# Kernel optimization log

Measured on AMD Instinct MI355X. Metric: run time of the kernel, lower is better.

Reference implementation:

```python
import jax, jax.numpy as jnp
import numpy as np

B, N, H = 128, 2048, 768
MAX_ANS = 15
NUM_ANS = MAX_ANS + 1  # default ans_to_aid = {str(i): i for i in range(16)}
LN_EPS = 1e-5


def setup_inputs() -> dict:
    key = jax.random.key(0)
    ks = jax.random.split(key, 7)
    s1 = 1.0 / np.sqrt(H)
    s2 = 1.0 / np.sqrt(2 * H)
    return {
        "v_emb": jax.random.normal(ks[0], (B, N, H), dtype=jnp.float32),
        "W1": jax.random.uniform(ks[1], (H, 2 * H), jnp.float32, -s1, s1),
        "b1": jax.random.uniform(ks[2], (2 * H,), jnp.float32, -s1, s1),
        "gamma": jnp.ones((2 * H,), jnp.float32),
        "beta": jnp.zeros((2 * H,), jnp.float32),
        "W2": jax.random.uniform(ks[3], (2 * H, 1), jnp.float32, -s2, s2),
        "b2": jax.random.uniform(ks[4], (1,), jnp.float32, -s2, s2),
    }


def _mlp(v_emb, W1, b1, gamma, beta, W2, b2):
    pooled = jnp.mean(v_emb, axis=1)                      # [B, H]
    h = jnp.dot(pooled, W1) + b1                          # [B, 2H]
    h = jax.nn.gelu(h, approximate=False)                 # torch nn.GELU() exact
    mu = jnp.mean(h, axis=-1, keepdims=True)
    var = jnp.mean((h - mu) ** 2, axis=-1, keepdims=True)
    h = (h - mu) * jax.lax.rsqrt(var + LN_EPS) * gamma + beta
    pred = jnp.dot(h, W2) + b2                            # [B, 1]
    return pred


def _pred_to_logits(pred):
    # vectorized round + clamp + one-hot (replaces per-sample .item() loop)
    aid = jnp.clip(jnp.round(pred[:, 0]), 0, MAX_ANS).astype(jnp.int32)
    return jax.nn.one_hot(aid, NUM_ANS, dtype=jnp.float32)  # [B, NUM_ANS]


def reference(v_emb, W1, b1, gamma, beta, W2, b2):
    pred = _mlp(v_emb, W1, b1, gamma, beta, W2, b2)
    logits = _pred_to_logits(pred)
    return pred, logits
```

## Files before the change

kernel.cpp:

```cpp
#include <hip/hip_runtime.h>
#include <cstdint>
#include <cstddef>

#define BB 128
#define NN 2048
#define HH 768
#define H2 1536
#define SSPLIT 16
#define CHUNK (NN / SSPLIT)
#define RT 16

__global__ __launch_bounds__(192) void pool_kernel(const float* __restrict__ v,
                                                   float* __restrict__ pooled) {
    const int b = blockIdx.x, s = blockIdx.y, t = threadIdx.x;
    const float4* vp =
        reinterpret_cast<const float4*>(v + ((size_t)b * NN + (size_t)s * CHUNK) * HH) + t;
    float4 acc = make_float4(0.f, 0.f, 0.f, 0.f);
#pragma unroll 4
    for (int n = 0; n < CHUNK; ++n) {
        float4 x = vp[(size_t)n * (HH / 4)];
        acc.x += x.x; acc.y += x.y; acc.z += x.z; acc.w += x.w;
    }
    float* p = pooled + (size_t)b * HH + t * 4;
    atomicAdd(p + 0, acc.x);
    atomicAdd(p + 1, acc.y);
    atomicAdd(p + 2, acc.z);
    atomicAdd(p + 3, acc.w);
}

__global__ __launch_bounds__(256) void mlp1_kernel(const float* __restrict__ pooled,
                                                   const float* __restrict__ W1,
                                                   const float* __restrict__ b1,
                                                   float* __restrict__ hbuf) {
    __shared__ float lds[RT * HH];
    const int j0 = blockIdx.x * 256, r0 = blockIdx.y * RT, tid = threadIdx.x;
    const float invN = 1.0f / (float)NN;

    const float4* src = reinterpret_cast<const float4*>(pooled + (size_t)r0 * HH);
    float4* dst = reinterpret_cast<float4*>(lds);
    for (int i = tid; i < RT * HH / 4; i += 256) {
        float4 x = src[i];
        x.x *= invN; x.y *= invN; x.z *= invN; x.w *= invN;
        dst[i] = x;
    }
    __syncthreads();

    const int j = j0 + tid;
    float acc[RT];
#pragma unroll
    for (int r = 0; r < RT; ++r) acc[r] = 0.f;

    const float* w = W1 + j;
    for (int k = 0; k < HH; k += 4) {
        const float w0 = w[(size_t)(k + 0) * H2];
        const float w1 = w[(size_t)(k + 1) * H2];
        const float w2 = w[(size_t)(k + 2) * H2];
        const float w3 = w[(size_t)(k + 3) * H2];
#pragma unroll
        for (int r = 0; r < RT; ++r) {
            float4 p = dst[(r * HH + k) >> 2];
            acc[r] = fmaf(p.x, w0, acc[r]);
            acc[r] = fmaf(p.y, w1, acc[r]);
            acc[r] = fmaf(p.z, w2, acc[r]);
            acc[r] = fmaf(p.w, w3, acc[r]);
        }
    }

    const float bj = b1[j];
#pragma unroll
    for (int r = 0; r < RT; ++r) {
        float hv = acc[r] + bj;
        float g = 0.5f * hv * (1.0f + erff(hv * 0.70710678118654752f));
        hbuf[(size_t)(r0 + r) * H2 + j] = g;
    }
}

__device__ inline float block_sum(float v, float* sbuf, int tid) {
#pragma unroll
    for (int off = 32; off > 0; off >>= 1) v += __shfl_down(v, off, 64);
    if ((tid & 63) == 0) sbuf[tid >> 6] = v;
    __syncthreads();
    if (tid == 0) sbuf[0] = sbuf[0] + sbuf[1] + sbuf[2] + sbuf[3];
    __syncthreads();
    float r = sbuf[0];
    __syncthreads();
    return r;
}

__global__ __launch_bounds__(256) void head_kernel(const float* __restrict__ hbuf,
                                                   const float* __restrict__ gamma,
                                                   const float* __restrict__ beta,
                                                   const float* __restrict__ W2,
                                                   const float* __restrict__ b2,
                                                   float* __restrict__ out) {
    __shared__ float sbuf[4];
    __shared__ int said;
    const int b = blockIdx.x, tid = threadIdx.x;
    const float* row = hbuf + (size_t)b * H2;

    float v[6];
#pragma unroll
    for (int i = 0; i < 6; ++i) v[i] = row[tid + i * 256];

    float s = 0.f;
#pragma unroll
    for (int i = 0; i < 6; ++i) s += v[i];
    const float mu = block_sum(s, sbuf, tid) * (1.0f / (float)H2);

    float sq = 0.f;
#pragma unroll
    for (int i = 0; i < 6; ++i) {
        float d = v[i] - mu;
        sq = fmaf(d, d, sq);
    }
    const float var = block_sum(sq, sbuf, tid) * (1.0f / (float)H2);
    const float rstd = rsqrtf(var + 1e-5f);

    float d = 0.f;
#pragma unroll
    for (int i = 0; i < 6; ++i) {
        int j = tid + i * 256;
        float y = (v[i] - mu) * rstd * gamma[j] + beta[j];
        d = fmaf(y, W2[j], d);
    }
    const float pred = block_sum(d, sbuf, tid) + b2[0];

    if (tid == 0) {
        out[b] = pred;
        float a = rintf(pred);
        a = fminf(fmaxf(a, 0.0f), 15.0f);
        said = (int)a;
    }
    __syncthreads();
    if (tid < 16) out[BB + b * 16 + tid] = (tid == said) ? 1.0f : 0.0f;
}

extern "C" void kernel_launch(void* const* d_in, const int* in_sizes, int n_in,
                              void* d_out, int out_size, void* d_ws, size_t ws_size,
                              hipStream_t stream) {
    const float* v_emb = (const float*)d_in[0];
    const float* W1    = (const float*)d_in[1];
    const float* b1    = (const float*)d_in[2];
    const float* gamma = (const float*)d_in[3];
    const float* beta  = (const float*)d_in[4];
    const float* W2    = (const float*)d_in[5];
    const float* b2    = (const float*)d_in[6];
    float* out = (float*)d_out;

    float* pooled = (float*)d_ws;
    float* hbuf   = pooled + (size_t)BB * HH;

    hipMemsetAsync(d_ws, 0, (size_t)BB * HH * sizeof(float), stream);

    pool_kernel<<<dim3(BB, SSPLIT), 192, 0, stream>>>(v_emb, pooled);
    mlp1_kernel<<<dim3(H2 / 256, BB / RT), 256, 0, stream>>>(pooled, W1, b1, hbuf);
    head_kernel<<<BB, 256, 0, stream>>>(hbuf, gamma, beta, W2, b2, out);
}
```

Measured before the change: 1.120 ms.

## Retile MLP1 to two columns per thread over fewer rows per block

Changes the first dense layer's tiling so each block covers 2 rows and 512 output columns, with each thread computing two columns. The grid grows from 48 blocks to 192 to raise parallelism on the weight-streaming GEMV. The mean scaling moves into the pooling kernel's atomic adds, and the pool loop unroll rises to 8. The trade-off is that W1 is now re-read by many more row blocks, which adds L2 traffic.

```diff
diff --git a/kernel.cpp b/kernel.cpp
--- a/kernel.cpp
+++ b/kernel.cpp
@@ -8,7 +8,8 @@
 #define H2 1536
 #define SSPLIT 16
 #define CHUNK (NN / SSPLIT)
-#define RT 16
+#define RT 2
+#define JT 512
 
 __global__ __launch_bounds__(192) void pool_kernel(const float* __restrict__ v,
                                                    float* __restrict__ pooled) {
@@ -16,62 +17,70 @@
     const float4* vp =
         reinterpret_cast<const float4*>(v + ((size_t)b * NN + (size_t)s * CHUNK) * HH) + t;
     float4 acc = make_float4(0.f, 0.f, 0.f, 0.f);
-#pragma unroll 4
+#pragma unroll 8
     for (int n = 0; n < CHUNK; ++n) {
         float4 x = vp[(size_t)n * (HH / 4)];
         acc.x += x.x; acc.y += x.y; acc.z += x.z; acc.w += x.w;
     }
+    const float invN = 1.0f / (float)NN;
     float* p = pooled + (size_t)b * HH + t * 4;
-    atomicAdd(p + 0, acc.x);
-    atomicAdd(p + 1, acc.y);
-    atomicAdd(p + 2, acc.z);
-    atomicAdd(p + 3, acc.w);
+    atomicAdd(p + 0, acc.x * invN);
+    atomicAdd(p + 1, acc.y * invN);
+    atomicAdd(p + 2, acc.z * invN);
+    atomicAdd(p + 3, acc.w * invN);
 }
 
 __global__ __launch_bounds__(256) void mlp1_kernel(const float* __restrict__ pooled,
                                                    const float* __restrict__ W1,
                                                    const float* __restrict__ b1,
                                                    float* __restrict__ hbuf) {
-    __shared__ float lds[RT * HH];
-    const int j0 = blockIdx.x * 256, r0 = blockIdx.y * RT, tid = threadIdx.x;
-    const float invN = 1.0f / (float)NN;
+    __shared__ float4 lds[RT * HH / 4];
+    const int j0 = blockIdx.x * JT, r0 = blockIdx.y * RT, tid = threadIdx.x;
 
     const float4* src = reinterpret_cast<const float4*>(pooled + (size_t)r0 * HH);
-    float4* dst = reinterpret_cast<float4*>(lds);
-    for (int i = tid; i < RT * HH / 4; i += 256) {
-        float4 x = src[i];
-        x.x *= invN; x.y *= invN; x.z *= invN; x.w *= invN;
-        dst[i] = x;
-    }
+    for (int i = tid; i < RT * HH / 4; i += 256) lds[i] = src[i];
     __syncthreads();
 
-    const int j = j0 + tid;
-    float acc[RT];
+    const int ja = j0 + tid;
+    const int jb = ja + 256;
+    float acca[RT], accb[RT];
 #pragma unroll
-    for (int r = 0; r < RT; ++r) acc[r] = 0.f;
+    for (int r = 0; r < RT; ++r) { acca[r] = 0.f; accb[r] = 0.f; }
 
-    const float* w = W1 + j;
+    const float* wa = W1 + ja;
+    const float* wb = W1 + jb;
     for (int k = 0; k < HH; k += 4) {
-        const float w0 = w[(size_t)(k + 0) * H2];
-        const float w1 = w[(size_t)(k + 1) * H2];
-        const float w2 = w[(size_t)(k + 2) * H2];
-        const float w3 = w[(size_t)(k + 3) * H2];
+        const float wa0 = wa[(size_t)(k + 0) * H2];
+        const float wa1 = wa[(size_t)(k + 1) * H2];
+        const float wa2 = wa[(size_t)(k + 2) * H2];
+        const float wa3 = wa[(size_t)(k + 3) * H2];
+        const float wb0 = wb[(size_t)(k + 0) * H2];
+        const float wb1 = wb[(size_t)(k + 1) * H2];
+        const float wb2 = wb[(size_t)(k + 2) * H2];
+        const float wb3 = wb[(size_t)(k + 3) * H2];
 #pragma unroll
         for (int r = 0; r < RT; ++r) {
-            float4 p = dst[(r * HH + k) >> 2];
-            acc[r] = fmaf(p.x, w0, acc[r]);
-            acc[r] = fmaf(p.y, w1, acc[r]);
-            acc[r] = fmaf(p.z, w2, acc[r]);
-            acc[r] = fmaf(p.w, w3, acc[r]);
+            float4 p = lds[r * (HH / 4) + (k >> 2)];
+            acca[r] = fmaf(p.x, wa0, acca[r]);
+            acca[r] = fmaf(p.y, wa1, acca[r]);
+            acca[r] = fmaf(p.z, wa2, acca[r]);
+            acca[r] = fmaf(p.w, wa3, acca[r]);
+            accb[r] = fmaf(p.x, wb0, accb[r]);
+            accb[r] = fmaf(p.y, wb1, accb[r]);
+            accb[r] = fmaf(p.z, wb2, accb[r]);
+            accb[r] = fmaf(p.w, wb3, accb[r]);
         }
     }
 
-    const float bj = b1[j];
+    const float ba = b1[ja], bb = b1[jb];
 #pragma unroll
     for (int r = 0; r < RT; ++r) {
-        float hv = acc[r] + bj;
-        float g = 0.5f * hv * (1.0f + erff(hv * 0.70710678118654752f));
-        hbuf[(size_t)(r0 + r) * H2 + j] = g;
+        float ha = acca[r] + ba;
+        float hb = accb[r] + bb;
+        float ga = 0.5f * ha * (1.0f + erff(ha * 0.70710678118654752f));
+        float gb = 0.5f * hb * (1.0f + erff(hb * 0.70710678118654752f));
+        hbuf[(size_t)(r0 + r) * H2 + ja] = ga;
+        hbuf[(size_t)(r0 + r) * H2 + jb] = gb;
     }
 }
 
@@ -153,6 +162,6 @@
     hipMemsetAsync(d_ws, 0, (size_t)BB * HH * sizeof(float), stream);
 
     pool_kernel<<<dim3(BB, SSPLIT), 192, 0, stream>>>(v_emb, pooled);
-    mlp1_kernel<<<dim3(H2 / 256, BB / RT), 256, 0, stream>>>(pooled, W1, b1, hbuf);
+    mlp1_kernel<<<dim3(H2 / JT, BB / RT), 256, 0, stream>>>(pooled, W1, b1, hbuf);
     head_kernel<<<BB, 256, 0, stream>>>(hbuf, gamma, beta, W2, b2, out);
 }
```

Measured after the change: 1.074 ms. -4.1%, faster.
